# Kernel optimization log

Measured on AMD Instinct MI355X. Metric: run time of the kernel, lower is better.

## Reference

```python
import jax, jax.numpy as jnp
import numpy as np

N = 50000      # nodes
E = 800000     # edges (before self loops)
F_IN = 128     # input feature dim
H = 4          # attention heads
C = 64         # per-head channels (hidden_dim = out_channels = 64)
HC = H * C     # 256, concat output width of each GATv2Conv
G = 32         # number of graphs in the batch
NEG_SLOPE_ATT = 0.2   # GATv2 internal LeakyReLU
NEG_SLOPE_ACT = 0.01  # encoder nn.LeakyReLU() default


def _glorot(key, shape, fan_in):
    return jax.random.normal(key, shape, jnp.float32) * (1.0 / np.sqrt(fan_in))


def setup_inputs() -> dict:
    key = jax.random.key(0)
    ks = jax.random.split(key, 32)
    inp = {}
    inp["x"] = jax.random.normal(ks[0], (N, F_IN), jnp.float32)
    inp["edge_index"] = jax.random.randint(ks[1], (2, E), 0, N, jnp.int32)
    inp["batch"] = jnp.sort(jax.random.randint(ks[2], (N,), 0, G, jnp.int32))
    i = 3
    for li, fin in ((1, F_IN), (2, HC), (3, HC)):
        inp[f"Wl{li}"] = _glorot(ks[i], (HC, fin), fin); i += 1
        inp[f"bl{li}"] = jnp.zeros((HC,), jnp.float32)
        inp[f"Wr{li}"] = _glorot(ks[i], (HC, fin), fin); i += 1
        inp[f"br{li}"] = jnp.zeros((HC,), jnp.float32)
        inp[f"att{li}"] = _glorot(ks[i], (H, C), C); i += 1
        inp[f"bo{li}"] = jnp.zeros((HC,), jnp.float32)
    return inp


def _gatv2_layer(x, src, dst, Wl, bl, Wr, br, att, bo):
    n = x.shape[0]
    xl = (x @ Wl.T + bl).reshape(n, H, C)  # source transform
    xr = (x @ Wr.T + br).reshape(n, H, C)  # target transform
    # per-edge attention logits: a^T LeakyReLU(xl[j] + xr[i])
    e = jax.nn.leaky_relu(xl[src] + xr[dst], negative_slope=NEG_SLOPE_ATT)  # [E', H, C]
    score = jnp.einsum('ehc,hc->eh', e, att)                                # [E', H]
    # segment softmax over incoming edges of each destination node
    m = jax.ops.segment_max(score, dst, num_segments=n)
    p = jnp.exp(score - m[dst])
    s = jax.ops.segment_sum(p, dst, num_segments=n)
    alpha = p / s[dst]
    out = jax.ops.segment_sum(alpha[:, :, None] * xl[src], dst, num_segments=n)
    return out.reshape(n, HC) + bo


def reference(x, edge_index, batch,
              Wl1, bl1, Wr1, br1, att1, bo1,
              Wl2, bl2, Wr2, br2, att2, bo2,
              Wl3, bl3, Wr3, br3, att3, bo3):
    loop = jnp.arange(N, dtype=edge_index.dtype)
    src = jnp.concatenate([edge_index[0], loop])  # add self loops (PyG default)
    dst = jnp.concatenate([edge_index[1], loop])
    h = _gatv2_layer(x, src, dst, Wl1, bl1, Wr1, br1, att1, bo1)
    h = jax.nn.leaky_relu(h, negative_slope=NEG_SLOPE_ACT)
    h = _gatv2_layer(h, src, dst, Wl2, bl2, Wr2, br2, att2, bo2)
    h = jax.nn.leaky_relu(h, negative_slope=NEG_SLOPE_ACT)
    h = _gatv2_layer(h, src, dst, Wl3, bl3, Wr3, br3, att3, bo3)
    # global mean pool over graphs
    sums = jax.ops.segment_sum(h, batch, num_segments=G)
    cnt = jax.ops.segment_sum(jnp.ones((N,), h.dtype), batch, num_segments=G)
    return sums / jnp.maximum(cnt, 1.0)[:, None]
```

## Files before the change

### kernel.cpp

```cpp
#include <hip/hip_runtime.h>

#define HEADS 4
#define CH 64
#define HC 256
#define NGRAPH 32
#define NEG_ATT 0.2f
#define NEG_ACT 0.01f

typedef __attribute__((ext_vector_type(8))) short bf16x8;
typedef __attribute__((ext_vector_type(4))) float f32x4;
typedef __attribute__((ext_vector_type(2))) float f32x2;

typedef __attribute__((address_space(3))) unsigned int lds_u32;
typedef const __attribute__((address_space(1))) unsigned int glob_u32;

__device__ __forceinline__ void gl_lds16(const void* g, void* l) {
  __builtin_amdgcn_global_load_lds((glob_u32*)(uintptr_t)g,
                                   (lds_u32*)(unsigned int)(uintptr_t)l, 16, 0, 0);
}

__device__ __forceinline__ void split2(float a, float b, unsigned& hi, unsigned& lo) {
  unsigned ua = __float_as_uint(a), ub = __float_as_uint(b);
  float la = a - __uint_as_float(ua & 0xFFFF0000u);
  float lb = b - __uint_as_float(ub & 0xFFFF0000u);
  hi = __builtin_amdgcn_perm(ub, ua, 0x07060302u);
  lo = __builtin_amdgcn_perm(__float_as_uint(lb), __float_as_uint(la), 0x07060302u);
}

__device__ __forceinline__ unsigned rtn_bf16(float f) {
  unsigned u = __float_as_uint(f);
  return (u + 0x7FFFu + ((u >> 16) & 1u)) >> 16;
}
__device__ __forceinline__ unsigned rtn_pack2(float a, float b) {
  return (rtn_bf16(b) << 16) | rtn_bf16(a);
}

__global__ __launch_bounds__(256) void convert_x(
    const float* __restrict__ X, unsigned short* __restrict__ xhi,
    unsigned short* __restrict__ xlo, int total4) {
  int g = blockIdx.x * 256 + threadIdx.x;
  if (g >= total4) return;
  float4 v = *(const float4*)&X[(size_t)g * 4];
  uint2 h2, l2;
  split2(v.x, v.y, h2.x, l2.x);
  split2(v.z, v.w, h2.y, l2.y);
  *(uint2*)&xhi[(size_t)g * 4] = h2;
  *(uint2*)&xlo[(size_t)g * 4] = l2;
}

__device__ __forceinline__ void conv_w_one(
    int g, const float* Wl, const float* Wr, int K,
    unsigned short* wfhi, unsigned short* wflo) {
  int lane = g & 63;
  int ct = (g >> 6) & 31;
  int kb = g >> 11;
  int col = ct * 16 + (lane & 15);
  int k = kb * 32 + (lane >> 4) * 8;
  const float* src = (col < HC) ? &Wl[(size_t)col * K + k] : &Wr[(size_t)(col - HC) * K + k];
  float4 v0 = *(const float4*)src;
  float4 v1 = *(const float4*)(src + 4);
  uint4 hq, lq;
  split2(v0.x, v0.y, hq.x, lq.x);
  split2(v0.z, v0.w, hq.y, lq.y);
  split2(v1.x, v1.y, hq.z, lq.z);
  split2(v1.z, v1.w, hq.w, lq.w);
  *(uint4*)&wfhi[(size_t)g * 8] = hq;
  *(uint4*)&wflo[(size_t)g * 8] = lq;
}

__global__ __launch_bounds__(256) void convert_w_all(
    const float* __restrict__ Wl1, const float* __restrict__ Wr1,
    unsigned short* __restrict__ w1hi, unsigned short* __restrict__ w1lo,
    const float* __restrict__ Wl2, const float* __restrict__ Wr2,
    unsigned short* __restrict__ w2hi, unsigned short* __restrict__ w2lo,
    const float* __restrict__ Wl3, const float* __restrict__ Wr3,
    unsigned short* __restrict__ w3hi, unsigned short* __restrict__ w3lo) {
  int g = blockIdx.x * 256 + threadIdx.x;
  if (g < 8192) conv_w_one(g, Wl1, Wr1, 128, w1hi, w1lo);
  else if (g < 8192 + 16384) conv_w_one(g - 8192, Wl2, Wr2, 256, w2hi, w2lo);
  else conv_w_one(g - 8192 - 16384, Wl3, Wr3, 256, w3hi, w3lo);
}

template <int K>
__global__ __launch_bounds__(256) void gemm_fused(
    const unsigned short* __restrict__ xhi, const unsigned short* __restrict__ xlo,
    const unsigned short* __restrict__ wfhi, const unsigned short* __restrict__ wflo,
    const float* __restrict__ bl, const float* __restrict__ br,
    unsigned short* __restrict__ Y1, unsigned short* __restrict__ Y2, int N, int nrb) {
  constexpr int nkb = K >> 5;
  __shared__ unsigned short Ah[2][128][32];
  __shared__ unsigned short Al[2][128][32];

  const int f = blockIdx.x;
  const int rb = (f & 7) + 8 * (f >> 5);
  const int cb = (f >> 3) & 3;
  if (rb >= nrb) return;

  const int tid = threadIdx.x;
  const int wave = tid >> 6;
  const int lane = tid & 63;
  const int quad = lane >> 4;
  const int l16 = lane & 15;
  const int wr = (wave >> 1) * 64;
  const int wc = (wave & 1) * 64;
  const int row0 = rb * 128;
  const int col0 = cb * 128;
  const int ctg0 = cb * 8 + (wave & 1) * 4;

  const int c0 = tid, c1 = tid + 256;
  const int r0g = row0 + (c0 >> 2), r1g = row0 + (c1 >> 2);
  const int ko0 = (c0 & 3) * 8, ko1 = (c1 & 3) * 8;
  const int gr0 = (r0g < N) ? r0g : N - 1;
  const int gr1 = (r1g < N) ? r1g : N - 1;

  f32x4 acc[4][4];
#pragma unroll
  for (int i = 0; i < 4; i++)
#pragma unroll
    for (int j = 0; j < 4; j++) acc[i][j] = (f32x4){0.f, 0.f, 0.f, 0.f};

  {
    size_t ga0 = (size_t)gr0 * K + ko0;
    size_t ga1 = (size_t)gr1 * K + ko1;
    gl_lds16(&xhi[ga0], &Ah[0][c0 >> 2][ko0]);
    gl_lds16(&xlo[ga0], &Al[0][c0 >> 2][ko0]);
    gl_lds16(&xhi[ga1], &Ah[0][c1 >> 2][ko1]);
    gl_lds16(&xlo[ga1], &Al[0][c1 >> 2][ko1]);
  }

#pragma unroll
  for (int kb = 0; kb < nkb; kb++) {
    const int cur = kb & 1, nxt = cur ^ 1;
    bf16x8 bhi[4], blo[4];
#pragma unroll
    for (int j = 0; j < 4; j++) {
      size_t ci = ((size_t)kb * 32 + ctg0 + j) * 64 + lane;
      bhi[j] = *(const bf16x8*)&wfhi[ci * 8];
      blo[j] = *(const bf16x8*)&wflo[ci * 8];
    }
    __syncthreads();
    if (kb + 1 < nkb) {
      int k0 = (kb + 1) * 32;
      size_t ga0 = (size_t)gr0 * K + k0 + ko0;
      size_t ga1 = (size_t)gr1 * K + k0 + ko1;
      gl_lds16(&xhi[ga0], &Ah[nxt][c0 >> 2][ko0]);
      gl_lds16(&xlo[ga0], &Al[nxt][c0 >> 2][ko0]);
      gl_lds16(&xhi[ga1], &Ah[nxt][c1 >> 2][ko1]);
      gl_lds16(&xlo[ga1], &Al[nxt][c1 >> 2][ko1]);
    }
    bf16x8 ahi[4], alo[4];
#pragma unroll
    for (int i = 0; i < 4; i++) {
      ahi[i] = *(const bf16x8*)&Ah[cur][wr + i * 16 + l16][quad * 8];
      alo[i] = *(const bf16x8*)&Al[cur][wr + i * 16 + l16][quad * 8];
    }
#pragma unroll
    for (int i = 0; i < 4; i++)
#pragma unroll
      for (int j = 0; j < 4; j++) {
        acc[i][j] = __builtin_amdgcn_mfma_f32_16x16x32_bf16(ahi[i], bhi[j], acc[i][j], 0, 0, 0);
        acc[i][j] = __builtin_amdgcn_mfma_f32_16x16x32_bf16(ahi[i], blo[j], acc[i][j], 0, 0, 0);
        acc[i][j] = __builtin_amdgcn_mfma_f32_16x16x32_bf16(alo[i], bhi[j], acc[i][j], 0, 0, 0);
      }
  }

#pragma unroll
  for (int j = 0; j < 4; j++) {
    int colg = col0 + wc + j * 16 + l16;
    unsigned short* Yp = (colg < HC) ? Y1 : Y2;
    int cc = (colg < HC) ? colg : colg - HC;
    float bv = (colg < HC) ? bl[cc] : br[cc];
#pragma unroll
    for (int i = 0; i < 4; i++)
#pragma unroll
      for (int r = 0; r < 4; r++) {
        int row = row0 + wr + i * 16 + quad * 4 + r;
        if (row < N)
          Yp[(size_t)row * HC + cc] = (unsigned short)rtn_bf16(acc[i][j][r] + bv);
      }
  }
}

__global__ __launch_bounds__(256) void hist_dst(
    const int* __restrict__ edst, int* __restrict__ counts, int E) {
  int e = blockIdx.x * 256 + threadIdx.x;
  if (e < E) atomicAdd(&counts[edst[e]], 1);
}

__global__ __launch_bounds__(256) void scan_blocks(
    const int* __restrict__ counts, int* __restrict__ row_start,
    int* __restrict__ bsum, int N) {
  __shared__ int tmp[256];
  int t = threadIdx.x;
  int base = blockIdx.x * 1024 + t * 4;
  int v0 = (base     < N) ? counts[base]     + 1 : 0;
  int v1 = (base + 1 < N) ? counts[base + 1] + 1 : 0;
  int v2 = (base + 2 < N) ? counts[base + 2] + 1 : 0;
  int v3 = (base + 3 < N) ? counts[base + 3] + 1 : 0;
  int c1 = v0 + v1, c2 = c1 + v2, tot = c2 + v3;
  tmp[t] = tot;
  __syncthreads();
  for (int off = 1; off < 256; off <<= 1) {
    int add = (t >= off) ? tmp[t - off] : 0;
    __syncthreads();
    tmp[t] += add;
    __syncthreads();
  }
  int excl = tmp[t] - tot;
  if (base     < N) row_start[base + 1] = excl + v0;
  if (base + 1 < N) row_start[base + 2] = excl + c1;
  if (base + 2 < N) row_start[base + 3] = excl + c2;
  if (base + 3 < N) row_start[base + 4] = excl + tot;
  if (t == 255) bsum[blockIdx.x] = tmp[255];
  if (blockIdx.x == 0 && t == 0) row_start[0] = 0;
}

__global__ void scan_tops(int* __restrict__ bsum, int nb) {
  int lane = threadIdx.x;
  int v = (lane < nb) ? bsum[lane] : 0;
  for (int off = 1; off < 64; off <<= 1) {
    int u = __shfl_up(v, off);
    if (lane >= off) v += u;
  }
  if (lane < nb) bsum[lane] = v;
}

__global__ __launch_bounds__(256) void scan_add(
    int* __restrict__ row_start, const int* __restrict__ bsum, int N) {
  int off = bsum[blockIdx.x];
  int i = (blockIdx.x + 1) * 1024 + threadIdx.x * 4;
#pragma unroll
  for (int k = 0; k < 4; k++)
    if (i + k < N) row_start[i + k + 1] += off;
}

__global__ __launch_bounds__(256) void csr_init(
    const int* __restrict__ row_start, int* __restrict__ fill_pos,
    int* __restrict__ csr_src, int N) {
  int i = blockIdx.x * 256 + threadIdx.x;
  if (i < N) {
    int p = row_start[i];
    csr_src[p] = i << 9;
    fill_pos[i] = p + 1;
  }
}

__global__ __launch_bounds__(256) void csr_scatter(
    const int* __restrict__ esrc, const int* __restrict__ edst,
    int* __restrict__ fill_pos, int* __restrict__ csr_src, int E) {
  int e = blockIdx.x * 256 + threadIdx.x;
  if (e < E) {
    int p = atomicAdd(&fill_pos[edst[e]], 1);
    csr_src[p] = esrc[e] << 9;
  }
}

__device__ __forceinline__ void unpk8(uint4 q, f32x2& v0, f32x2& v1, f32x2& v2, f32x2& v3) {
  v0.x = __uint_as_float(q.x << 16); v0.y = __uint_as_float(q.x & 0xFFFF0000u);
  v1.x = __uint_as_float(q.y << 16); v1.y = __uint_as_float(q.y & 0xFFFF0000u);
  v2.x = __uint_as_float(q.z << 16); v2.y = __uint_as_float(q.z & 0xFFFF0000u);
  v3.x = __uint_as_float(q.w << 16); v3.y = __uint_as_float(q.w & 0xFFFF0000u);
}

__device__ __forceinline__ float edge8(uint4 q,
    f32x2 r0, f32x2 r1, f32x2 r2, f32x2 r3,
    f32x2 a0, f32x2 a1, f32x2 a2, f32x2 a3,
    f32x2& l0, f32x2& l1, f32x2& l2, f32x2& l3) {
  unpk8(q, l0, l1, l2, l3);
  f32x2 t0 = l0 + r0, t1 = l1 + r1, t2 = l2 + r2, t3 = l3 + r3;
  f32x2 u0 = t0 * NEG_ATT, u1 = t1 * NEG_ATT, u2 = t2 * NEG_ATT, u3 = t3 * NEG_ATT;
  t0.x = fmaxf(t0.x, u0.x); t0.y = fmaxf(t0.y, u0.y);
  t1.x = fmaxf(t1.x, u1.x); t1.y = fmaxf(t1.y, u1.y);
  t2.x = fmaxf(t2.x, u2.x); t2.y = fmaxf(t2.y, u2.y);
  t3.x = fmaxf(t3.x, u3.x); t3.y = fmaxf(t3.y, u3.y);
  f32x2 dv = t0 * a0;
  dv = t1 * a1 + dv;
  dv = t2 * a2 + dv;
  dv = t3 * a3 + dv;
  float d = dv.x + dv.y;
  d += __shfl_xor(d, 1);
  d += __shfl_xor(d, 2);
  d += __shfl_xor(d, 4);
  return d;
}

__global__ __launch_bounds__(256) void gat_fused(
    const unsigned short* __restrict__ xl, const unsigned short* __restrict__ xr,
    const int* __restrict__ row_start, const int* __restrict__ csr_soff,
    const float* __restrict__ att, const float* __restrict__ bo,
    unsigned short* __restrict__ ohi, unsigned short* __restrict__ olo,
    int N, int mode) {
  int dst = (blockIdx.x * 256 + threadIdx.x) >> 6;
  int lane = threadIdx.x & 63;
  if (dst >= N) return;
  const int slot = lane >> 5;
  const int c8 = (lane & 31) * 8;
  const int loff = c8 * 2;
  const char* xlc = (const char*)xl;

  f32x2 a0 = *(const f32x2*)&att[c8 + 0];
  f32x2 a1 = *(const f32x2*)&att[c8 + 2];
  f32x2 a2 = *(const f32x2*)&att[c8 + 4];
  f32x2 a3 = *(const f32x2*)&att[c8 + 6];

  uint4 qr = *(const uint4*)((const char*)xr + (size_t)dst * 512 + loff);
  f32x2 r0, r1, r2, r3;
  unpk8(qr, r0, r1, r2, r3);

  f32x2 o0 = {0.f, 0.f}, o1 = {0.f, 0.f}, o2 = {0.f, 0.f}, o3 = {0.f, 0.f};
  float s = 0.f;
  int p = row_start[dst];
  const int end = row_start[dst + 1];

  for (; p + 4 <= end; p += 4) {
    int iA = csr_soff[p + slot];
    int iB = csr_soff[p + 2 + slot];
    uint4 qA = *(const uint4*)(xlc + iA + loff);
    uint4 qB = *(const uint4*)(xlc + iB + loff);
    f32x2 lA0, lA1, lA2, lA3, lB0, lB1, lB2, lB3;
    float dA = edge8(qA, r0, r1, r2, r3, a0, a1, a2, a3, lA0, lA1, lA2, lA3);
    float dB = edge8(qB, r0, r1, r2, r3, a0, a1, a2, a3, lB0, lB1, lB2, lB3);
    float eA = __expf(dA);
    float eB = __expf(dB);
    s += eA + eB;
    o0 = lA0 * eA + o0; o0 = lB0 * eB + o0;
    o1 = lA1 * eA + o1; o1 = lB1 * eB + o1;
    o2 = lA2 * eA + o2; o2 = lB2 * eB + o2;
    o3 = lA3 * eA + o3; o3 = lB3 * eB + o3;
  }
  for (; p < end; p += 2) {
    int i = p + slot;
    bool vld = i < end;
    int ii = vld ? i : end - 1;
    uint4 q = *(const uint4*)(xlc + csr_soff[ii] + loff);
    f32x2 l0, l1, l2, l3;
    float d = edge8(q, r0, r1, r2, r3, a0, a1, a2, a3, l0, l1, l2, l3);
    float pe = vld ? __expf(d) : 0.f;
    s += pe;
    o0 = l0 * pe + o0;
    o1 = l1 * pe + o1;
    o2 = l2 * pe + o2;
    o3 = l3 * pe + o3;
  }

  s += __shfl_xor(s, 32);
  o0.x += __shfl_xor(o0.x, 32); o0.y += __shfl_xor(o0.y, 32);
  o1.x += __shfl_xor(o1.x, 32); o1.y += __shfl_xor(o1.y, 32);
  o2.x += __shfl_xor(o2.x, 32); o2.y += __shfl_xor(o2.y, 32);
  o3.x += __shfl_xor(o3.x, 32); o3.y += __shfl_xor(o3.y, 32);

  if (slot != 0) return;
  float inv = 1.f / s;
  f32x2 b0 = *(const f32x2*)&bo[c8 + 0];
  f32x2 b1 = *(const f32x2*)&bo[c8 + 2];
  f32x2 b2 = *(const f32x2*)&bo[c8 + 4];
  f32x2 b3 = *(const f32x2*)&bo[c8 + 6];
  f32x2 s0 = o0 * inv + b0;
  f32x2 s1 = o1 * inv + b1;
  f32x2 s2 = o2 * inv + b2;
  f32x2 s3 = o3 * inv + b3;
  if (mode == 1) {
    f32x2 w0 = s0 * NEG_ACT, w1 = s1 * NEG_ACT, w2 = s2 * NEG_ACT, w3 = s3 * NEG_ACT;
    s0.x = fmaxf(s0.x, w0.x); s0.y = fmaxf(s0.y, w0.y);
    s1.x = fmaxf(s1.x, w1.x); s1.y = fmaxf(s1.y, w1.y);
    s2.x = fmaxf(s2.x, w2.x); s2.y = fmaxf(s2.y, w2.y);
    s3.x = fmaxf(s3.x, w3.x); s3.y = fmaxf(s3.y, w3.y);
    uint4 hq, lq;
    split2(s0.x, s0.y, hq.x, lq.x);
    split2(s1.x, s1.y, hq.y, lq.y);
    split2(s2.x, s2.y, hq.z, lq.z);
    split2(s3.x, s3.y, hq.w, lq.w);
    *(uint4*)&ohi[(size_t)dst * HC + c8] = hq;
    *(uint4*)&olo[(size_t)dst * HC + c8] = lq;
  } else {
    uint4 pk;
    pk.x = rtn_pack2(s0.x, s0.y);
    pk.y = rtn_pack2(s1.x, s1.y);
    pk.z = rtn_pack2(s2.x, s2.y);
    pk.w = rtn_pack2(s3.x, s3.y);
    *(uint4*)&ohi[(size_t)dst * HC + c8] = pk;
  }
}

__global__ __launch_bounds__(256) void pool_partial(
    const unsigned short* __restrict__ h3, const int* __restrict__ batch,
    float* __restrict__ out, int* __restrict__ cnt, int N) {
  __shared__ float part[NGRAPH][HC];
  __shared__ int bsh[256];
  __shared__ int cpart[NGRAPH];
  int j = threadIdx.x;
#pragma unroll
  for (int g = 0; g < NGRAPH; g++) part[g][j] = 0.f;
  if (j < NGRAPH) cpart[j] = 0;
  int n0 = blockIdx.x * 256;
  int nend = min(n0 + 256, N);
  int nj = n0 + j;
  bsh[j] = (nj < N) ? batch[nj] : 0;
  __syncthreads();
  if (nj < nend) atomicAdd(&cpart[bsh[j]], 1);
  for (int n = n0; n < nend; n++) {
    int g = bsh[n - n0];
    unsigned q = h3[(size_t)n * HC + j];
    part[g][j] += __uint_as_float(q << 16);
  }
  __syncthreads();
#pragma unroll
  for (int g = 0; g < NGRAPH; g++) {
    float v = part[g][j];
    if (v != 0.f) atomicAdd(&out[g * HC + j], v);
  }
  if (j < NGRAPH && cpart[j] > 0) atomicAdd(&cnt[j], cpart[j]);
}

__global__ __launch_bounds__(256) void pool_final(
    float* __restrict__ out, const int* __restrict__ cnt) {
  int g = blockIdx.x;
  int j = threadIdx.x;
  float c = (float)max(cnt[g], 1);
  out[g * HC + j] /= c;
}

extern "C" void kernel_launch(void* const* d_in, const int* in_sizes, int n_in,
                              void* d_out, int out_size, void* d_ws, size_t ws_size,
                              hipStream_t stream) {
  const float* x = (const float*)d_in[0];
  const int* ei = (const int*)d_in[1];
  const int* batch = (const int*)d_in[2];
  const int N = in_sizes[2];
  const int E = in_sizes[1] / 2;
  const int Etot = E + N;

  const float* Wl[3] = {(const float*)d_in[3], (const float*)d_in[9], (const float*)d_in[15]};
  const float* bl[3] = {(const float*)d_in[4], (const float*)d_in[10], (const float*)d_in[16]};
  const float* Wr[3] = {(const float*)d_in[5], (const float*)d_in[11], (const float*)d_in[17]};
  const float* br[3] = {(const float*)d_in[6], (const float*)d_in[12], (const float*)d_in[18]};
  const float* att[3] = {(const float*)d_in[7], (const float*)d_in[13], (const float*)d_in[19]};
  const float* bo[3] = {(const float*)d_in[8], (const float*)d_in[14], (const float*)d_in[20]};

  float* B0 = (float*)d_ws;
  float* B1 = B0 + (size_t)N * HC;
  float* B2 = B1 + (size_t)N * HC;
  unsigned short* w1hi = (unsigned short*)(B2 + (size_t)N * HC);
  unsigned short* w1lo = w1hi + 512 * 128;
  unsigned short* w2hi = w1lo + 512 * 128;
  unsigned short* w2lo = w2hi + 512 * 256;
  unsigned short* w3hi = w2lo + 512 * 256;
  unsigned short* w3lo = w3hi + 512 * 256;
  int* counts = (int*)(w3lo + 512 * 256);
  int* row_start = counts + N;
  int* bsum = row_start + N + 1;
  int* fill_pos = bsum + 64;
  int* csr_src = fill_pos + N;
  int* cnt = csr_src + Etot;

  unsigned short* xlB = (unsigned short*)B1;
  unsigned short* xrB = (unsigned short*)B2;
  unsigned short* xhiL1 = (unsigned short*)B0;
  unsigned short* xloL1 = xhiL1 + (size_t)N * 128;
  unsigned short* xhiL = (unsigned short*)B0;
  unsigned short* xloL = xhiL + (size_t)N * HC;
  unsigned short* h3B = (unsigned short*)B0;

  const int* esrc = ei;
  const int* edst = ei + E;

  convert_x<<<(N * 128 / 4 + 255) / 256, 256, 0, stream>>>(x, xhiL1, xloL1, N * 128 / 4);
  convert_w_all<<<(8192 + 16384 + 16384) / 256, 256, 0, stream>>>(
      Wl[0], Wr[0], w1hi, w1lo, Wl[1], Wr[1], w2hi, w2lo, Wl[2], Wr[2], w3hi, w3lo);

  const int nscan = (N + 1023) / 1024;
  (void)hipMemsetAsync(counts, 0, (size_t)N * sizeof(int), stream);
  hist_dst<<<(E + 255) / 256, 256, 0, stream>>>(edst, counts, E);
  scan_blocks<<<nscan, 256, 0, stream>>>(counts, row_start, bsum, N);
  scan_tops<<<1, 64, 0, stream>>>(bsum, nscan);
  scan_add<<<nscan - 1, 256, 0, stream>>>(row_start, bsum, N);
  csr_init<<<(N + 255) / 256, 256, 0, stream>>>(row_start, fill_pos, csr_src, N);
  csr_scatter<<<(E + 255) / 256, 256, 0, stream>>>(esrc, edst, fill_pos, csr_src, E);

  const int nrb = (N + 127) / 128;
  const int gblocks = ((nrb + 7) / 8) * 32;
  const int fblocks = (N * 64 + 255) / 256;

  gemm_fused<128><<<gblocks, 256, 0, stream>>>(xhiL1, xloL1, w1hi, w1lo, bl[0], br[0], xlB, xrB, N, nrb);
  gat_fused<<<fblocks, 256, 0, stream>>>(xlB, xrB, row_start, csr_src, att[0], bo[0],
                                         xhiL, xloL, N, 1);
  gemm_fused<256><<<gblocks, 256, 0, stream>>>(xhiL, xloL, w2hi, w2lo, bl[1], br[1], xlB, xrB, N, nrb);
  gat_fused<<<fblocks, 256, 0, stream>>>(xlB, xrB, row_start, csr_src, att[1], bo[1],
                                         xhiL, xloL, N, 1);
  gemm_fused<256><<<gblocks, 256, 0, stream>>>(xhiL, xloL, w3hi, w3lo, bl[2], br[2], xlB, xrB, N, nrb);
  gat_fused<<<fblocks, 256, 0, stream>>>(xlB, xrB, row_start, csr_src, att[2], bo[2],
                                         h3B, nullptr, N, 2);

  (void)hipMemsetAsync(d_out, 0, NGRAPH * HC * sizeof(float), stream);
  (void)hipMemsetAsync(cnt, 0, NGRAPH * sizeof(int), stream);
  pool_partial<<<(N + 255) / 256, 256, 0, stream>>>(h3B, batch, (float*)d_out, cnt, N);
  pool_final<<<NGRAPH, 256, 0, stream>>>((float*)d_out, cnt);
}
```

Measured before the change: 643.1 us.

## Merge setup kernels and unroll GAT edge loop to eight edges

Folds the x and weight conversions into one kernel and merges the two memsets into one. The top-level scan is now recomputed redundantly per block inside scan_add, and CSR init and scatter are combined into one kernel using a separate zeroed counter. This cuts the number of small kernel launches and the dependency bubbles between them. The GAT aggregation loop also gains an 8-edge unrolled body so more gathers are in flight per iteration, at the cost of more registers per thread.

```diff
diff --git a/kernel.cpp b/kernel.cpp
--- a/kernel.cpp
+++ b/kernel.cpp
@@ -33,19 +33,6 @@
 }
 __device__ __forceinline__ unsigned rtn_pack2(float a, float b) {
   return (rtn_bf16(b) << 16) | rtn_bf16(a);
-}
-
-__global__ __launch_bounds__(256) void convert_x(
-    const float* __restrict__ X, unsigned short* __restrict__ xhi,
-    unsigned short* __restrict__ xlo, int total4) {
-  int g = blockIdx.x * 256 + threadIdx.x;
-  if (g >= total4) return;
-  float4 v = *(const float4*)&X[(size_t)g * 4];
-  uint2 h2, l2;
-  split2(v.x, v.y, h2.x, l2.x);
-  split2(v.z, v.w, h2.y, l2.y);
-  *(uint2*)&xhi[(size_t)g * 4] = h2;
-  *(uint2*)&xlo[(size_t)g * 4] = l2;
 }
 
 __device__ __forceinline__ void conv_w_one(
@@ -68,7 +55,9 @@
   *(uint4*)&wflo[(size_t)g * 8] = lq;
 }
 
-__global__ __launch_bounds__(256) void convert_w_all(
+__global__ __launch_bounds__(256) void convert_all(
+    const float* __restrict__ X, unsigned short* __restrict__ xhi,
+    unsigned short* __restrict__ xlo, int total4,
     const float* __restrict__ Wl1, const float* __restrict__ Wr1,
     unsigned short* __restrict__ w1hi, unsigned short* __restrict__ w1lo,
     const float* __restrict__ Wl2, const float* __restrict__ Wr2,
@@ -76,9 +65,19 @@
     const float* __restrict__ Wl3, const float* __restrict__ Wr3,
     unsigned short* __restrict__ w3hi, unsigned short* __restrict__ w3lo) {
   int g = blockIdx.x * 256 + threadIdx.x;
-  if (g < 8192) conv_w_one(g, Wl1, Wr1, 128, w1hi, w1lo);
-  else if (g < 8192 + 16384) conv_w_one(g - 8192, Wl2, Wr2, 256, w2hi, w2lo);
-  else conv_w_one(g - 8192 - 16384, Wl3, Wr3, 256, w3hi, w3lo);
+  if (g < total4) {
+    float4 v = *(const float4*)&X[(size_t)g * 4];
+    uint2 h2, l2;
+    split2(v.x, v.y, h2.x, l2.x);
+    split2(v.z, v.w, h2.y, l2.y);
+    *(uint2*)&xhi[(size_t)g * 4] = h2;
+    *(uint2*)&xlo[(size_t)g * 4] = l2;
+  } else {
+    int h = g - total4;
+    if (h < 8192) conv_w_one(h, Wl1, Wr1, 128, w1hi, w1lo);
+    else if (h < 24576) conv_w_one(h - 8192, Wl2, Wr2, 256, w2hi, w2lo);
+    else if (h < 40960) conv_w_one(h - 24576, Wl3, Wr3, 256, w3hi, w3lo);
+  }
 }
 
 template <int K>
@@ -215,42 +214,37 @@
   if (blockIdx.x == 0 && t == 0) row_start[0] = 0;
 }
 
-__global__ void scan_tops(int* __restrict__ bsum, int nb) {
-  int lane = threadIdx.x;
-  int v = (lane < nb) ? bsum[lane] : 0;
-  for (int off = 1; off < 64; off <<= 1) {
-    int u = __shfl_up(v, off);
-    if (lane >= off) v += u;
-  }
-  if (lane < nb) bsum[lane] = v;
-}
-
-__global__ __launch_bounds__(256) void scan_add(
-    int* __restrict__ row_start, const int* __restrict__ bsum, int N) {
-  int off = bsum[blockIdx.x];
-  int i = (blockIdx.x + 1) * 1024 + threadIdx.x * 4;
+__global__ __launch_bounds__(256) void scan_finish(
+    int* __restrict__ row_start, const int* __restrict__ bsum, int N, int nb) {
+  __shared__ int s_off;
+  const int c = blockIdx.x + 1;
+  if (threadIdx.x < 64) {
+    int v = ((int)threadIdx.x < nb) ? bsum[threadIdx.x] : 0;
+    for (int off = 1; off < 64; off <<= 1) {
+      int u = __shfl_up(v, off);
+      if ((int)threadIdx.x >= off) v += u;
+    }
+    if ((int)threadIdx.x == c - 1) s_off = v;
+  }
+  __syncthreads();
+  int off = s_off;
+  int i = c * 1024 + threadIdx.x * 4;
 #pragma unroll
   for (int k = 0; k < 4; k++)
     if (i + k < N) row_start[i + k + 1] += off;
 }
 
-__global__ __launch_bounds__(256) void csr_init(
-    const int* __restrict__ row_start, int* __restrict__ fill_pos,
-    int* __restrict__ csr_src, int N) {
+__global__ __launch_bounds__(256) void csr_build(
+    const int* __restrict__ esrc, const int* __restrict__ edst,
+    const int* __restrict__ row_start, int* __restrict__ fpos2,
+    int* __restrict__ csr_src, int N, int E) {
   int i = blockIdx.x * 256 + threadIdx.x;
   if (i < N) {
-    int p = row_start[i];
-    csr_src[p] = i << 9;
-    fill_pos[i] = p + 1;
-  }
-}
-
-__global__ __launch_bounds__(256) void csr_scatter(
-    const int* __restrict__ esrc, const int* __restrict__ edst,
-    int* __restrict__ fill_pos, int* __restrict__ csr_src, int E) {
-  int e = blockIdx.x * 256 + threadIdx.x;
-  if (e < E) {
-    int p = atomicAdd(&fill_pos[edst[e]], 1);
+    csr_src[row_start[i]] = i << 9;
+  } else if (i < N + E) {
+    int e = i - N;
+    int d = edst[e];
+    int p = row_start[d] + 1 + atomicAdd(&fpos2[d], 1);
     csr_src[p] = esrc[e] << 9;
   }
 }
@@ -312,6 +306,31 @@
   int p = row_start[dst];
   const int end = row_start[dst + 1];
 
+  for (; p + 8 <= end; p += 8) {
+    int iA = csr_soff[p + 0 + slot];
+    int iB = csr_soff[p + 2 + slot];
+    int iC = csr_soff[p + 4 + slot];
+    int iD = csr_soff[p + 6 + slot];
+    uint4 qA = *(const uint4*)(xlc + iA + loff);
+    uint4 qB = *(const uint4*)(xlc + iB + loff);
+    uint4 qC = *(const uint4*)(xlc + iC + loff);
+    uint4 qD = *(const uint4*)(xlc + iD + loff);
+    f32x2 lA0, lA1, lA2, lA3, lB0, lB1, lB2, lB3;
+    f32x2 lC0, lC1, lC2, lC3, lD0, lD1, lD2, lD3;
+    float dA = edge8(qA, r0, r1, r2, r3, a0, a1, a2, a3, lA0, lA1, lA2, lA3);
+    float dB = edge8(qB, r0, r1, r2, r3, a0, a1, a2, a3, lB0, lB1, lB2, lB3);
+    float dC = edge8(qC, r0, r1, r2, r3, a0, a1, a2, a3, lC0, lC1, lC2, lC3);
+    float dD = edge8(qD, r0, r1, r2, r3, a0, a1, a2, a3, lD0, lD1, lD2, lD3);
+    float eA = __expf(dA);
+    float eB = __expf(dB);
+    float eC = __expf(dC);
+    float eD = __expf(dD);
+    s += (eA + eB) + (eC + eD);
+    o0 = lA0 * eA + o0; o0 = lB0 * eB + o0; o0 = lC0 * eC + o0; o0 = lD0 * eD + o0;
+    o1 = lA1 * eA + o1; o1 = lB1 * eB + o1; o1 = lC1 * eC + o1; o1 = lD1 * eD + o1;
+    o2 = lA2 * eA + o2; o2 = lB2 * eB + o2; o2 = lC2 * eC + o2; o2 = lD2 * eD + o2;
+    o3 = lA3 * eA + o3; o3 = lB3 * eB + o3; o3 = lC3 * eC + o3; o3 = lD3 * eD + o3;
+  }
   for (; p + 4 <= end; p += 4) {
     int iA = csr_soff[p + slot];
     int iB = csr_soff[p + 2 + slot];
@@ -447,10 +466,10 @@
   unsigned short* w3hi = w2lo + 512 * 256;
   unsigned short* w3lo = w3hi + 512 * 256;
   int* counts = (int*)(w3lo + 512 * 256);
-  int* row_start = counts + N;
+  int* fpos2 = counts + N;
+  int* row_start = fpos2 + N;
   int* bsum = row_start + N + 1;
-  int* fill_pos = bsum + 64;
-  int* csr_src = fill_pos + N;
+  int* csr_src = bsum + 64;
   int* cnt = csr_src + Etot;
 
   unsigned short* xlB = (unsigned short*)B1;
@@ -464,18 +483,17 @@
   const int* esrc = ei;
   const int* edst = ei + E;
 
-  convert_x<<<(N * 128 / 4 + 255) / 256, 256, 0, stream>>>(x, xhiL1, xloL1, N * 128 / 4);
-  convert_w_all<<<(8192 + 16384 + 16384) / 256, 256, 0, stream>>>(
+  (void)hipMemsetAsync(counts, 0, (size_t)2 * N * sizeof(int), stream);
+  const int total4 = N * 128 / 4;
+  convert_all<<<(total4 + 40960 + 255) / 256, 256, 0, stream>>>(
+      x, xhiL1, xloL1, total4,
       Wl[0], Wr[0], w1hi, w1lo, Wl[1], Wr[1], w2hi, w2lo, Wl[2], Wr[2], w3hi, w3lo);
 
   const int nscan = (N + 1023) / 1024;
-  (void)hipMemsetAsync(counts, 0, (size_t)N * sizeof(int), stream);
   hist_dst<<<(E + 255) / 256, 256, 0, stream>>>(edst, counts, E);
   scan_blocks<<<nscan, 256, 0, stream>>>(counts, row_start, bsum, N);
-  scan_tops<<<1, 64, 0, stream>>>(bsum, nscan);
-  scan_add<<<nscan - 1, 256, 0, stream>>>(row_start, bsum, N);
-  csr_init<<<(N + 255) / 256, 256, 0, stream>>>(row_start, fill_pos, csr_src, N);
-  csr_scatter<<<(E + 255) / 256, 256, 0, stream>>>(esrc, edst, fill_pos, csr_src, E);
+  scan_finish<<<nscan - 1, 256, 0, stream>>>(row_start, bsum, N, nscan);
+  csr_build<<<(N + E + 255) / 256, 256, 0, stream>>>(esrc, edst, row_start, fpos2, csr_src, N, E);
 
   const int nrb = (N + 127) / 128;
   const int gblocks = ((nrb + 7) / 8) * 32;
```

After: 665.7 us. +3.5%, slower.
